# Kernel optimization log

Measured on AMD Instinct MI355X. Metric: run time of the kernel, lower is better.

The kernel has to match this reference:

```python
import jax, jax.numpy as jnp
import numpy as np


def _knn_idx(xyz_bn3, k):
    # dist[b,i,j] = ||x_i - x_j||^2 over the point cloud.
    # Faithful to the source: torch.topk defaults to largest=True, so the
    # k+1 LARGEST distances are selected and index 0 (the farthest) is dropped.
    sq = jnp.sum(xyz_bn3 ** 2, axis=-1)  # [b, n]
    dist = sq[:, :, None] + sq[:, None, :] - 2.0 * jnp.einsum('bic,bjc->bij', xyz_bn3, xyz_bn3)
    _, idx = jax.lax.top_k(dist, k + 1)  # largest, sorted descending -> [b, n, k+1]
    return idx[:, :, 1:]  # drop slot 0, keep k neighbors -> [b, n, k]


def setup_inputs() -> dict:
    key = jax.random.key(0)
    B, N, C, K, NB = 8, 4096, 128, 20, 3
    ks = jax.random.split(key, 4)
    scale = 1.0 / np.sqrt(C).astype(np.float32)
    xyz = jax.random.normal(ks[0], (B, 3, N), jnp.float32)
    points = jax.random.normal(ks[1], (B, C, N), jnp.float32)
    W1 = jax.random.normal(ks[2], (NB, C, C), jnp.float32) * scale  # convs[2i] 1x1 kernels
    b1 = jnp.zeros((NB, C), jnp.float32)
    W2 = jax.random.normal(ks[3], (NB, C, C), jnp.float32) * scale  # convs[2i+1] 1x1 kernels
    b2 = jnp.zeros((NB, C), jnp.float32)
    return {"xyz": xyz, "points": points, "W1": W1, "b1": b1, "W2": W2, "b2": b2, "k": K}


def reference(xyz, points, W1, b1, W2, b2, k):
    # xyz: [b, 3, n]; points: [b, C, n]; W1/W2: [n_blocks, C, C]; b1/b2: [n_blocks, C]
    n_blocks = W1.shape[0]
    xyz_bn3 = jnp.transpose(xyz, (0, 2, 1))  # [b, n, 3]
    for i in range(n_blocks):
        shortcut = points
        p = jax.nn.leaky_relu(points, 0.01)  # elementwise, layout [b, C, n]
        # center branch: 1x1 conv == per-point linear
        center = jnp.einsum('oc,bcn->bon', W1[i], p) + b1[i][None, :, None]  # [b, C, n]
        if i == 0:
            idx = _knn_idx(xyz_bn3, k)  # [b, n, k], int32
            # grouping_operation gather: grouped[b,c,n,j] = p[b,c, idx[b,n,j]]
            grouped = jax.vmap(lambda pb, ib: pb[:, ib])(p, idx)  # [b, C, n, k]
            gnn = jnp.einsum('oc,bcnk->bonk', W2[i], grouped) + b2[i][None, :, None, None]
            # mean over concat([center(1 slot), gnn(k slots)], slot axis)
            agg = (center + jnp.sum(gnn, axis=-1)) / (k + 1)
        else:
            # later blocks: grouped_points is just the center point itself (K=1)
            gnn = jnp.einsum('oc,bcn->bon', W2[i], p) + b2[i][None, :, None]
            agg = (center + gnn) * 0.5
        points = agg + shortcut
    return points
```

## Files before the change

kernel.cpp:

```cpp
#include <hip/hip_runtime.h>
#include <math.h>

#define B 8
#define N 4096
#define C 128
#define K 20
#define M (B*N)

__device__ __forceinline__ float lrelu(float x) { return x > 0.f ? x : 0.01f * x; }

__global__ void prep_w(const float* __restrict__ W1, const float* __restrict__ b1,
                       const float* __restrict__ W2, const float* __restrict__ b2,
                       float* __restrict__ wt, float* __restrict__ bias) {
    int t = blockIdx.x * blockDim.x + threadIdx.x;
    if (t < C * C) {
        int c = t / C, o = t % C;
        int oc = o * C + c;
        wt[0 * C * C + t] = W1[oc] * (1.f / 21.f);
        wt[1 * C * C + t] = W2[oc] * (1.f / 21.f);
        wt[2 * C * C + t] = (W1[1 * C * C + oc] + W2[1 * C * C + oc]) * 0.5f;
        wt[3 * C * C + t] = (W1[2 * C * C + oc] + W2[2 * C * C + oc]) * 0.5f;
    }
    if (t < C) {
        bias[t]         = (b1[t] + 20.f * b2[t]) * (1.f / 21.f);
        bias[C + t]     = (b1[C + t] + b2[C + t]) * 0.5f;
        bias[2 * C + t] = (b1[2 * C + t] + b2[2 * C + t]) * 0.5f;
    }
}

__global__ void prep_xyz(const float* __restrict__ xyz, float4* __restrict__ xt) {
    int t = blockIdx.x * blockDim.x + threadIdx.x;
    if (t >= B * N) return;
    int b = t >> 12, n = t & (N - 1);
    const float* p = xyz + (size_t)b * 3 * N;
    float x = p[n], y = p[N + n], z = p[2 * N + n];
    xt[t] = make_float4(x, y, z, x * x + y * y + z * z);
}

__global__ __launch_bounds__(256) void transpose_rs(const float* __restrict__ in,
                                                    float* __restrict__ out, int R, int S) {
    __shared__ float tile[64][65];
    int b = blockIdx.z;
    int r0 = blockIdx.y * 64, s0 = blockIdx.x * 64;
    const float* pin = in + (size_t)b * R * S;
    float* pout = out + (size_t)b * R * S;
    int tr = threadIdx.x >> 4;
    int ts = (threadIdx.x & 15) << 2;
#pragma unroll
    for (int i = 0; i < 4; ++i) {
        int r = tr + i * 16;
        float4 v = *(const float4*)&pin[(size_t)(r0 + r) * S + s0 + ts];
        tile[r][ts + 0] = v.x; tile[r][ts + 1] = v.y;
        tile[r][ts + 2] = v.z; tile[r][ts + 3] = v.w;
    }
    __syncthreads();
#pragma unroll
    for (int i = 0; i < 4; ++i) {
        int s = tr + i * 16;
        float4 v = make_float4(tile[ts + 0][s], tile[ts + 1][s], tile[ts + 2][s], tile[ts + 3][s]);
        *(float4*)&pout[(size_t)(s0 + s) * R + r0 + ts] = v;
    }
}

__global__ __launch_bounds__(256, 4) void knn_kernel(const float4* __restrict__ xt,
                                                     int* __restrict__ idx) {
    __shared__ unsigned int wred[4][2];
    __shared__ float maxred[4][4];
    __shared__ unsigned int cnt[4];
    __shared__ unsigned long long cand[4][128];

    int tid = threadIdx.x;
    int wid = tid >> 6, lane = tid & 63;
    int blk = blockIdx.x;
    int b = blk >> 10;
    int i0 = (blk & 1023) << 2;
    const float4* xb = xt + (size_t)b * N;

    float4 xi[4];
#pragma unroll
    for (int r = 0; r < 4; ++r) xi[r] = xb[i0 + r];

    if (tid < 4) cnt[tid] = 0;

    float d[4][16];
    float mx[4] = {-1e30f, -1e30f, -1e30f, -1e30f};
#pragma unroll
    for (int u = 0; u < 16; ++u) {
        float4 xj = xb[u * 256 + tid];
#pragma unroll
        for (int r = 0; r < 4; ++r) {
            float dd = xi[r].w + xj.w - 2.f * (xi[r].x * xj.x + xi[r].y * xj.y + xi[r].z * xj.z);
            d[r][u] = dd;
            mx[r] = fmaxf(mx[r], dd);
        }
    }
#pragma unroll
    for (int off = 32; off; off >>= 1) {
#pragma unroll
        for (int r = 0; r < 4; ++r) mx[r] = fmaxf(mx[r], __shfl_xor(mx[r], off));
    }
    if (lane == 0) {
#pragma unroll
        for (int r = 0; r < 4; ++r) maxred[wid][r] = mx[r];
    }
    __syncthreads();

    float lo[4], hi[4], thr[4];
    bool done[4];
#pragma unroll
    for (int r = 0; r < 4; ++r) {
        hi[r] = fmaxf(fmaxf(maxred[0][r], maxred[1][r]), fmaxf(maxred[2][r], maxred[3][r]));
        lo[r] = 0.f;
        thr[r] = 0.f;
        done[r] = false;
    }

    for (int it = 0; it < 20; ++it) {
        if (done[0] && done[1] && done[2] && done[3]) break;
#pragma unroll
        for (int r = 0; r < 4; ++r) if (!done[r]) thr[r] = 0.5f * (lo[r] + hi[r]);
        unsigned int c[4] = {0u, 0u, 0u, 0u};
#pragma unroll
        for (int u = 0; u < 16; ++u) {
#pragma unroll
            for (int r = 0; r < 4; ++r) c[r] += (d[r][u] > thr[r]) ? 1u : 0u;
        }
        unsigned int p01 = c[0] | (c[1] << 16);
        unsigned int p23 = c[2] | (c[3] << 16);
#pragma unroll
        for (int off = 32; off; off >>= 1) {
            p01 += __shfl_xor(p01, off);
            p23 += __shfl_xor(p23, off);
        }
        if (lane == 0) { wred[wid][0] = p01; wred[wid][1] = p23; }
        __syncthreads();
        unsigned int s01 = wred[0][0] + wred[1][0] + wred[2][0] + wred[3][0];
        unsigned int s23 = wred[0][1] + wred[1][1] + wred[2][1] + wred[3][1];
        unsigned int cc[4] = { s01 & 0xFFFFu, s01 >> 16, s23 & 0xFFFFu, s23 >> 16 };
#pragma unroll
        for (int r = 0; r < 4; ++r) {
            if (!done[r]) {
                if (cc[r] >= (unsigned)(K + 1) && cc[r] <= 96u) done[r] = true;
                else if (cc[r] > 96u) lo[r] = thr[r];
                else hi[r] = thr[r];
            }
        }
        __syncthreads();
    }
#pragma unroll
    for (int r = 0; r < 4; ++r) if (!done[r]) thr[r] = lo[r];

#pragma unroll
    for (int u = 0; u < 16; ++u) {
#pragma unroll
        for (int r = 0; r < 4; ++r) {
            float dd = d[r][u];
            if (dd > thr[r]) {
                unsigned int pos = atomicAdd(&cnt[r], 1u);
                if (pos < 128u) {
                    unsigned int j = (unsigned)(u * 256 + tid);
                    cand[r][pos] = ((unsigned long long)__float_as_uint(dd) << 32) | (unsigned)(~j);
                }
            }
        }
    }
    __syncthreads();

    {
        int r = wid;
        unsigned int c = cnt[r]; if (c > 128u) c = 128u;
        for (int s = lane; s < (int)c; s += 64) {
            unsigned long long my = cand[r][s];
            int rank = 0;
            for (int q = 0; q < (int)c; ++q) rank += (cand[r][q] > my) ? 1 : 0;
            if (rank >= 1 && rank <= K) {
                int row = (b << 12) + i0 + r;
                idx[(size_t)row * K + (rank - 1)] = (int)(~(unsigned int)my);
            }
        }
    }
}

__global__ __launch_bounds__(256) void gather_sum(const float* __restrict__ pt,
                                                  const int* __restrict__ idx,
                                                  float* __restrict__ sT) {
    int t = blockIdx.x * 256 + threadIdx.x;
    int pnt = t >> 5;
    int c4 = (t & 31) << 2;
    int b = pnt >> 12;
    const float* pb = pt + (size_t)b * N * C;
    const int* ip = idx + (size_t)pnt * K;
    float4 acc = make_float4(0.f, 0.f, 0.f, 0.f);
#pragma unroll 4
    for (int k = 0; k < K; ++k) {
        int j = ip[k];
        float4 v = *(const float4*)&pb[(size_t)j * C + c4];
        acc.x += lrelu(v.x); acc.y += lrelu(v.y);
        acc.z += lrelu(v.z); acc.w += lrelu(v.w);
    }
    *(float4*)&sT[(size_t)pnt * C + c4] = acc;
}

__global__ __launch_bounds__(256) void gemm_fused(const float* __restrict__ A0,
                                                  const float* __restrict__ A1,
                                                  const float* __restrict__ Wt0,
                                                  const float* __restrict__ Wt1,
                                                  const float* __restrict__ bias,
                                                  const float* __restrict__ shortcut,
                                                  float* __restrict__ out) {
    __shared__ float As[64][17];
    __shared__ float Ws[16][128];
    int row0 = blockIdx.x * 64;
    int tid = threadIdx.x;
    int r_ld = tid >> 2;
    int c_ld = (tid & 3) << 2;
    int r0 = (tid >> 4) << 2;
    int o0 = (tid & 15) << 2;

    float acc[4][8];
#pragma unroll
    for (int j = 0; j < 4; ++j)
#pragma unroll
        for (int l = 0; l < 8; ++l) acc[j][l] = 0.f;

    for (int phase = 0; phase < 2; ++phase) {
        const float* A = phase ? A1 : A0;
        if (!A) break;
        const float* Wt = phase ? Wt1 : Wt0;
        for (int c0 = 0; c0 < C; c0 += 16) {
            float4 av = *(const float4*)&A[(size_t)(row0 + r_ld) * C + c0 + c_ld];
            if (phase == 0) {
                av.x = lrelu(av.x); av.y = lrelu(av.y);
                av.z = lrelu(av.z); av.w = lrelu(av.w);
            }
            As[r_ld][c_ld + 0] = av.x; As[r_ld][c_ld + 1] = av.y;
            As[r_ld][c_ld + 2] = av.z; As[r_ld][c_ld + 3] = av.w;
#pragma unroll
            for (int q = 0; q < 2; ++q) {
                int slot = tid + q * 256;
                int kk = slot >> 5;
                int oo = (slot & 31) << 2;
                *(float4*)&Ws[kk][oo] = *(const float4*)&Wt[(size_t)(c0 + kk) * C + oo];
            }
            __syncthreads();
#pragma unroll
            for (int kk = 0; kk < 16; ++kk) {
                float a0 = As[r0 + 0][kk], a1 = As[r0 + 1][kk];
                float a2 = As[r0 + 2][kk], a3 = As[r0 + 3][kk];
                float4 w0 = *(const float4*)&Ws[kk][o0];
                float4 w1 = *(const float4*)&Ws[kk][o0 + 64];
                acc[0][0] += a0 * w0.x; acc[0][1] += a0 * w0.y; acc[0][2] += a0 * w0.z; acc[0][3] += a0 * w0.w;
                acc[0][4] += a0 * w1.x; acc[0][5] += a0 * w1.y; acc[0][6] += a0 * w1.z; acc[0][7] += a0 * w1.w;
                acc[1][0] += a1 * w0.x; acc[1][1] += a1 * w0.y; acc[1][2] += a1 * w0.z; acc[1][3] += a1 * w0.w;
                acc[1][4] += a1 * w1.x; acc[1][5] += a1 * w1.y; acc[1][6] += a1 * w1.z; acc[1][7] += a1 * w1.w;
                acc[2][0] += a2 * w0.x; acc[2][1] += a2 * w0.y; acc[2][2] += a2 * w0.z; acc[2][3] += a2 * w0.w;
                acc[2][4] += a2 * w1.x; acc[2][5] += a2 * w1.y; acc[2][6] += a2 * w1.z; acc[2][7] += a2 * w1.w;
                acc[3][0] += a3 * w0.x; acc[3][1] += a3 * w0.y; acc[3][2] += a3 * w0.z; acc[3][3] += a3 * w0.w;
                acc[3][4] += a3 * w1.x; acc[3][5] += a3 * w1.y; acc[3][6] += a3 * w1.z; acc[3][7] += a3 * w1.w;
            }
            __syncthreads();
        }
    }

    float4 bb0 = *(const float4*)&bias[o0];
    float4 bb1 = *(const float4*)&bias[o0 + 64];
#pragma unroll
    for (int j = 0; j < 4; ++j) {
        size_t r = (size_t)(row0 + r0 + j);
        float4 s0 = *(const float4*)&shortcut[r * C + o0];
        float4 s1 = *(const float4*)&shortcut[r * C + o0 + 64];
        float4 v0 = make_float4(acc[j][0] + bb0.x + s0.x, acc[j][1] + bb0.y + s0.y,
                                acc[j][2] + bb0.z + s0.z, acc[j][3] + bb0.w + s0.w);
        float4 v1 = make_float4(acc[j][4] + bb1.x + s1.x, acc[j][5] + bb1.y + s1.y,
                                acc[j][6] + bb1.z + s1.z, acc[j][7] + bb1.w + s1.w);
        *(float4*)&out[r * C + o0] = v0;
        *(float4*)&out[r * C + o0 + 64] = v1;
    }
}

extern "C" void kernel_launch(void* const* d_in, const int* in_sizes, int n_in,
                              void* d_out, int out_size, void* d_ws, size_t ws_size,
                              hipStream_t stream) {
    const float* xyz    = (const float*)d_in[0];
    const float* points = (const float*)d_in[1];
    const float* W1     = (const float*)d_in[2];
    const float* b1     = (const float*)d_in[3];
    const float* W2     = (const float*)d_in[4];
    const float* b2     = (const float*)d_in[5];

    float* ws = (float*)d_ws;
    float4* xt  = (float4*)ws;
    float* pt_a = ws + (size_t)B * N * 4;
    float* pt_b = pt_a + (size_t)M * C;
    float* sT   = pt_b + (size_t)M * C;
    float* wt   = sT + (size_t)M * C;
    float* bias = wt + 4 * C * C;
    int*   idx  = (int*)(bias + 3 * C);

    prep_w<<<(C * C + 255) / 256, 256, 0, stream>>>(W1, b1, W2, b2, wt, bias);
    prep_xyz<<<(B * N + 255) / 256, 256, 0, stream>>>(xyz, xt);
    {
        dim3 g(N / 64, C / 64, B);
        transpose_rs<<<g, 256, 0, stream>>>(points, pt_a, C, N);
    }
    knn_kernel<<<M / 4, 256, 0, stream>>>(xt, idx);
    gather_sum<<<(M * 32) / 256, 256, 0, stream>>>(pt_a, idx, sT);
    gemm_fused<<<M / 64, 256, 0, stream>>>(pt_a, sT, wt, wt + C * C, bias, pt_a, pt_b);
    gemm_fused<<<M / 64, 256, 0, stream>>>(pt_b, nullptr, wt + 2 * C * C, nullptr, bias + C, pt_b, pt_a);
    gemm_fused<<<M / 64, 256, 0, stream>>>(pt_a, nullptr, wt + 3 * C * C, nullptr, bias + 2 * C, pt_a, pt_b);
    {
        dim3 g(C / 64, N / 64, B);
        transpose_rs<<<g, 256, 0, stream>>>(pt_b, (float*)d_out, N, C);
    }
}
```

Baseline: 218.8 us.

## Fuse GEMM blocks and output transpose, use ballot-based counting in kNN

Merges the two prep kernels into a single launch. In the kNN kernel, the bisection counting uses wave ballot/popcount with a double-buffered shared count array that drops one barrier per iteration, and candidate insertion does one atomic per wave using mbcnt instead of one per lane. Blocks 1 and 2 are fused into one kernel that keeps the 64-row tile in shared memory and writes the transposed output directly, which removes one GEMM launch, the final transpose, and their global round trips. Block 0 now stages its input tile once and reuses it for the shortcut. It also adds fallback index filling and index masking for safety, at the cost of more shared memory per block and possibly lower occupancy.

```diff
diff --git a/kernel.cpp b/kernel.cpp
--- a/kernel.cpp
+++ b/kernel.cpp
@@ -9,32 +9,32 @@
 
 __device__ __forceinline__ float lrelu(float x) { return x > 0.f ? x : 0.01f * x; }
 
-__global__ void prep_w(const float* __restrict__ W1, const float* __restrict__ b1,
-                       const float* __restrict__ W2, const float* __restrict__ b2,
-                       float* __restrict__ wt, float* __restrict__ bias) {
-    int t = blockIdx.x * blockDim.x + threadIdx.x;
-    if (t < C * C) {
-        int c = t / C, o = t % C;
+__global__ void prep_all(const float* __restrict__ xyz,
+                         const float* __restrict__ W1, const float* __restrict__ b1,
+                         const float* __restrict__ W2, const float* __restrict__ b2,
+                         float4* __restrict__ xt, float* __restrict__ wt,
+                         float* __restrict__ bias) {
+    int blk = blockIdx.x;
+    if (blk < 64) {
+        int t = blk * 256 + threadIdx.x;
+        int c = t >> 7, o = t & 127;
         int oc = o * C + c;
-        wt[0 * C * C + t] = W1[oc] * (1.f / 21.f);
-        wt[1 * C * C + t] = W2[oc] * (1.f / 21.f);
-        wt[2 * C * C + t] = (W1[1 * C * C + oc] + W2[1 * C * C + oc]) * 0.5f;
+        wt[t]             = W1[oc] * (1.f / 21.f);
+        wt[C * C + t]     = W2[oc] * (1.f / 21.f);
+        wt[2 * C * C + t] = (W1[C * C + oc] + W2[C * C + oc]) * 0.5f;
         wt[3 * C * C + t] = (W1[2 * C * C + oc] + W2[2 * C * C + oc]) * 0.5f;
-    }
-    if (t < C) {
-        bias[t]         = (b1[t] + 20.f * b2[t]) * (1.f / 21.f);
-        bias[C + t]     = (b1[C + t] + b2[C + t]) * 0.5f;
-        bias[2 * C + t] = (b1[2 * C + t] + b2[2 * C + t]) * 0.5f;
-    }
-}
-
-__global__ void prep_xyz(const float* __restrict__ xyz, float4* __restrict__ xt) {
-    int t = blockIdx.x * blockDim.x + threadIdx.x;
-    if (t >= B * N) return;
-    int b = t >> 12, n = t & (N - 1);
-    const float* p = xyz + (size_t)b * 3 * N;
-    float x = p[n], y = p[N + n], z = p[2 * N + n];
-    xt[t] = make_float4(x, y, z, x * x + y * y + z * z);
+        if (t < C) {
+            bias[t]         = (b1[t] + 20.f * b2[t]) * (1.f / 21.f);
+            bias[C + t]     = (b1[C + t] + b2[C + t]) * 0.5f;
+            bias[2 * C + t] = (b1[2 * C + t] + b2[2 * C + t]) * 0.5f;
+        }
+    } else {
+        int t = (blk - 64) * 256 + threadIdx.x;
+        int b = t >> 12, n = t & (N - 1);
+        const float* p = xyz + (size_t)b * 3 * N;
+        float x = p[n], y = p[N + n], z = p[2 * N + n];
+        xt[t] = make_float4(x, y, z, x * x + y * y + z * z);
+    }
 }
 
 __global__ __launch_bounds__(256) void transpose_rs(const float* __restrict__ in,
@@ -64,88 +64,85 @@
 
 __global__ __launch_bounds__(256, 4) void knn_kernel(const float4* __restrict__ xt,
                                                      int* __restrict__ idx) {
-    __shared__ unsigned int wred[4][2];
     __shared__ float maxred[4][4];
+    __shared__ unsigned int wcnt[2][4][4];
     __shared__ unsigned int cnt[4];
     __shared__ unsigned long long cand[4][128];
 
-    int tid = threadIdx.x;
-    int wid = tid >> 6, lane = tid & 63;
-    int blk = blockIdx.x;
-    int b = blk >> 10;
-    int i0 = (blk & 1023) << 2;
-    const float4* xb = xt + (size_t)b * N;
-
-    float4 xi[4];
-#pragma unroll
-    for (int r = 0; r < 4; ++r) xi[r] = xb[i0 + r];
-
+    const int tid = threadIdx.x;
+    const int wid = tid >> 6, lane = tid & 63;
+    const int blk = blockIdx.x;
+    const int b = blk >> 10;
+    const int i0 = (blk & 1023) << 2;
+    const float4* __restrict__ xb = xt + (size_t)b * N;
+
+    float4 xi0 = xb[i0 + 0], xi1 = xb[i0 + 1], xi2 = xb[i0 + 2], xi3 = xb[i0 + 3];
     if (tid < 4) cnt[tid] = 0;
 
     float d[4][16];
-    float mx[4] = {-1e30f, -1e30f, -1e30f, -1e30f};
+    float mx0 = -1e30f, mx1 = -1e30f, mx2 = -1e30f, mx3 = -1e30f;
 #pragma unroll
     for (int u = 0; u < 16; ++u) {
         float4 xj = xb[u * 256 + tid];
-#pragma unroll
-        for (int r = 0; r < 4; ++r) {
-            float dd = xi[r].w + xj.w - 2.f * (xi[r].x * xj.x + xi[r].y * xj.y + xi[r].z * xj.z);
-            d[r][u] = dd;
-            mx[r] = fmaxf(mx[r], dd);
-        }
+        float s0 = fmaf(xi0.x, xj.x, fmaf(xi0.y, xj.y, xi0.z * xj.z));
+        float s1 = fmaf(xi1.x, xj.x, fmaf(xi1.y, xj.y, xi1.z * xj.z));
+        float s2 = fmaf(xi2.x, xj.x, fmaf(xi2.y, xj.y, xi2.z * xj.z));
+        float s3 = fmaf(xi3.x, xj.x, fmaf(xi3.y, xj.y, xi3.z * xj.z));
+        float d0 = xi0.w + xj.w - 2.f * s0;
+        float d1 = xi1.w + xj.w - 2.f * s1;
+        float d2 = xi2.w + xj.w - 2.f * s2;
+        float d3 = xi3.w + xj.w - 2.f * s3;
+        d[0][u] = d0; d[1][u] = d1; d[2][u] = d2; d[3][u] = d3;
+        mx0 = fmaxf(mx0, d0); mx1 = fmaxf(mx1, d1);
+        mx2 = fmaxf(mx2, d2); mx3 = fmaxf(mx3, d3);
     }
 #pragma unroll
     for (int off = 32; off; off >>= 1) {
-#pragma unroll
-        for (int r = 0; r < 4; ++r) mx[r] = fmaxf(mx[r], __shfl_xor(mx[r], off));
+        mx0 = fmaxf(mx0, __shfl_xor(mx0, off));
+        mx1 = fmaxf(mx1, __shfl_xor(mx1, off));
+        mx2 = fmaxf(mx2, __shfl_xor(mx2, off));
+        mx3 = fmaxf(mx3, __shfl_xor(mx3, off));
     }
     if (lane == 0) {
-#pragma unroll
-        for (int r = 0; r < 4; ++r) maxred[wid][r] = mx[r];
+        maxred[wid][0] = mx0; maxred[wid][1] = mx1;
+        maxred[wid][2] = mx2; maxred[wid][3] = mx3;
     }
     __syncthreads();
 
-    float lo[4], hi[4], thr[4];
-    bool done[4];
+    float lo[4] = {0.f, 0.f, 0.f, 0.f};
+    float hi[4], thr[4];
+    bool done[4] = {false, false, false, false};
 #pragma unroll
     for (int r = 0; r < 4; ++r) {
         hi[r] = fmaxf(fmaxf(maxred[0][r], maxred[1][r]), fmaxf(maxred[2][r], maxred[3][r]));
-        lo[r] = 0.f;
         thr[r] = 0.f;
-        done[r] = false;
-    }
-
-    for (int it = 0; it < 20; ++it) {
-        if (done[0] && done[1] && done[2] && done[3]) break;
-#pragma unroll
-        for (int r = 0; r < 4; ++r) if (!done[r]) thr[r] = 0.5f * (lo[r] + hi[r]);
-        unsigned int c[4] = {0u, 0u, 0u, 0u};
-#pragma unroll
-        for (int u = 0; u < 16; ++u) {
-#pragma unroll
-            for (int r = 0; r < 4; ++r) c[r] += (d[r][u] > thr[r]) ? 1u : 0u;
-        }
-        unsigned int p01 = c[0] | (c[1] << 16);
-        unsigned int p23 = c[2] | (c[3] << 16);
-#pragma unroll
-        for (int off = 32; off; off >>= 1) {
-            p01 += __shfl_xor(p01, off);
-            p23 += __shfl_xor(p23, off);
-        }
-        if (lane == 0) { wred[wid][0] = p01; wred[wid][1] = p23; }
-        __syncthreads();
-        unsigned int s01 = wred[0][0] + wred[1][0] + wred[2][0] + wred[3][0];
-        unsigned int s23 = wred[0][1] + wred[1][1] + wred[2][1] + wred[3][1];
-        unsigned int cc[4] = { s01 & 0xFFFFu, s01 >> 16, s23 & 0xFFFFu, s23 >> 16 };
+    }
+
+    bool alldone = false;
+    for (int it = 0; it < 24 && !alldone; ++it) {
+        int p = it & 1;
 #pragma unroll
         for (int r = 0; r < 4; ++r) {
-            if (!done[r]) {
-                if (cc[r] >= (unsigned)(K + 1) && cc[r] <= 96u) done[r] = true;
-                else if (cc[r] > 96u) lo[r] = thr[r];
-                else hi[r] = thr[r];
-            }
-        }
-        __syncthreads();
+            if (done[r]) continue;
+            float t = 0.5f * (lo[r] + hi[r]);
+            thr[r] = t;
+            unsigned int cc = 0;
+#pragma unroll
+            for (int u = 0; u < 16; ++u)
+                cc += (unsigned int)__popcll(__ballot(d[r][u] > t));
+            if (lane == 0) wcnt[p][wid][r] = cc;
+        }
+        __syncthreads();
+        alldone = true;
+#pragma unroll
+        for (int r = 0; r < 4; ++r) {
+            if (done[r]) continue;
+            unsigned int tot = wcnt[p][0][r] + wcnt[p][1][r] + wcnt[p][2][r] + wcnt[p][3][r];
+            if (tot >= (unsigned)(K + 1) && tot <= 96u) done[r] = true;
+            else if (tot > 96u) lo[r] = thr[r];
+            else hi[r] = thr[r];
+            if (!done[r]) alldone = false;
+        }
     }
 #pragma unroll
     for (int r = 0; r < 4; ++r) if (!done[r]) thr[r] = lo[r];
@@ -154,12 +151,21 @@
     for (int u = 0; u < 16; ++u) {
 #pragma unroll
         for (int r = 0; r < 4; ++r) {
-            float dd = d[r][u];
-            if (dd > thr[r]) {
-                unsigned int pos = atomicAdd(&cnt[r], 1u);
-                if (pos < 128u) {
-                    unsigned int j = (unsigned)(u * 256 + tid);
-                    cand[r][pos] = ((unsigned long long)__float_as_uint(dd) << 32) | (unsigned)(~j);
+            bool pred = d[r][u] > thr[r];
+            unsigned long long m = __ballot(pred);
+            if (m) {
+                unsigned int base = 0;
+                if (lane == 0) base = atomicAdd(&cnt[r], (unsigned int)__popcll(m));
+                base = (unsigned int)__shfl((int)base, 0);
+                if (pred) {
+                    unsigned int bel = __builtin_amdgcn_mbcnt_lo((unsigned int)m, 0u);
+                    bel = __builtin_amdgcn_mbcnt_hi((unsigned int)(m >> 32), bel);
+                    unsigned int pos = base + bel;
+                    if (pos < 128u) {
+                        unsigned int j = (unsigned int)(u * 256 + tid);
+                        cand[r][pos] = ((unsigned long long)__float_as_uint(d[r][u]) << 32)
+                                       | (unsigned int)(~j);
+                    }
                 }
             }
         }
@@ -168,15 +174,16 @@
 
     {
         int r = wid;
+        int row = (b << 12) + i0 + r;
         unsigned int c = cnt[r]; if (c > 128u) c = 128u;
+        if (c < (unsigned)(K + 1) && lane < K)
+            idx[(size_t)row * K + lane] = (int)lane + 1;
         for (int s = lane; s < (int)c; s += 64) {
             unsigned long long my = cand[r][s];
             int rank = 0;
             for (int q = 0; q < (int)c; ++q) rank += (cand[r][q] > my) ? 1 : 0;
-            if (rank >= 1 && rank <= K) {
-                int row = (b << 12) + i0 + r;
+            if (rank >= 1 && rank <= K)
                 idx[(size_t)row * K + (rank - 1)] = (int)(~(unsigned int)my);
-            }
         }
     }
 }
@@ -193,7 +200,7 @@
     float4 acc = make_float4(0.f, 0.f, 0.f, 0.f);
 #pragma unroll 4
     for (int k = 0; k < K; ++k) {
-        int j = ip[k];
+        int j = ip[k] & (N - 1);
         float4 v = *(const float4*)&pb[(size_t)j * C + c4];
         acc.x += lrelu(v.x); acc.y += lrelu(v.y);
         acc.z += lrelu(v.z); acc.w += lrelu(v.w);
@@ -201,21 +208,90 @@
     *(float4*)&sT[(size_t)pnt * C + c4] = acc;
 }
 
-__global__ __launch_bounds__(256) void gemm_fused(const float* __restrict__ A0,
-                                                  const float* __restrict__ A1,
-                                                  const float* __restrict__ Wt0,
-                                                  const float* __restrict__ Wt1,
-                                                  const float* __restrict__ bias,
-                                                  const float* __restrict__ shortcut,
-                                                  float* __restrict__ out) {
-    __shared__ float As[64][17];
+__device__ __forceinline__ void stage_ws(const float* __restrict__ Wt, float (*Ws)[128],
+                                         int c0, int tid) {
+#pragma unroll
+    for (int q = 0; q < 2; ++q) {
+        int slot = q * 256 + tid;
+        int kk = slot >> 5, oo = (slot & 31) << 2;
+        *(float4*)&Ws[kk][oo] = *(const float4*)&Wt[(size_t)(c0 + kk) * C + oo];
+    }
+}
+
+template<bool LR>
+__device__ __forceinline__ void mm_tileP(const float (*P)[132], const float (*Ws)[128],
+                                         float acc[4][8], int r0, int o0, int c0) {
+#pragma unroll
+    for (int q = 0; q < 4; ++q) {
+        float4 aj[4];
+#pragma unroll
+        for (int j = 0; j < 4; ++j) {
+            float4 v = *(const float4*)&P[r0 + j][c0 + q * 4];
+            if (LR) { v.x = lrelu(v.x); v.y = lrelu(v.y); v.z = lrelu(v.z); v.w = lrelu(v.w); }
+            aj[j] = v;
+        }
+#pragma unroll
+        for (int kq = 0; kq < 4; ++kq) {
+            int kk = q * 4 + kq;
+            float4 w0 = *(const float4*)&Ws[kk][o0];
+            float4 w1 = *(const float4*)&Ws[kk][o0 + 64];
+#pragma unroll
+            for (int j = 0; j < 4; ++j) {
+                float a = (kq == 0) ? aj[j].x : (kq == 1) ? aj[j].y : (kq == 2) ? aj[j].z : aj[j].w;
+                acc[j][0] = fmaf(a, w0.x, acc[j][0]); acc[j][1] = fmaf(a, w0.y, acc[j][1]);
+                acc[j][2] = fmaf(a, w0.z, acc[j][2]); acc[j][3] = fmaf(a, w0.w, acc[j][3]);
+                acc[j][4] = fmaf(a, w1.x, acc[j][4]); acc[j][5] = fmaf(a, w1.y, acc[j][5]);
+                acc[j][6] = fmaf(a, w1.z, acc[j][6]); acc[j][7] = fmaf(a, w1.w, acc[j][7]);
+            }
+        }
+    }
+}
+
+__device__ __forceinline__ void mm_tileA(const float (*As)[20], const float (*Ws)[128],
+                                         float acc[4][8], int r0, int o0) {
+#pragma unroll
+    for (int q = 0; q < 4; ++q) {
+        float4 aj[4];
+#pragma unroll
+        for (int j = 0; j < 4; ++j)
+            aj[j] = *(const float4*)&As[r0 + j][q * 4];
+#pragma unroll
+        for (int kq = 0; kq < 4; ++kq) {
+            int kk = q * 4 + kq;
+            float4 w0 = *(const float4*)&Ws[kk][o0];
+            float4 w1 = *(const float4*)&Ws[kk][o0 + 64];
+#pragma unroll
+            for (int j = 0; j < 4; ++j) {
+                float a = (kq == 0) ? aj[j].x : (kq == 1) ? aj[j].y : (kq == 2) ? aj[j].z : aj[j].w;
+                acc[j][0] = fmaf(a, w0.x, acc[j][0]); acc[j][1] = fmaf(a, w0.y, acc[j][1]);
+                acc[j][2] = fmaf(a, w0.z, acc[j][2]); acc[j][3] = fmaf(a, w0.w, acc[j][3]);
+                acc[j][4] = fmaf(a, w1.x, acc[j][4]); acc[j][5] = fmaf(a, w1.y, acc[j][5]);
+                acc[j][6] = fmaf(a, w1.z, acc[j][6]); acc[j][7] = fmaf(a, w1.w, acc[j][7]);
+            }
+        }
+    }
+}
+
+__global__ __launch_bounds__(256) void gemm_block0(const float* __restrict__ A0,
+                                                   const float* __restrict__ A1,
+                                                   const float* __restrict__ Wt0,
+                                                   const float* __restrict__ Wt1,
+                                                   const float* __restrict__ bias0,
+                                                   float* __restrict__ out) {
+    __shared__ float P0[64][132];
+    __shared__ float As[64][20];
     __shared__ float Ws[16][128];
-    int row0 = blockIdx.x * 64;
-    int tid = threadIdx.x;
-    int r_ld = tid >> 2;
-    int c_ld = (tid & 3) << 2;
-    int r0 = (tid >> 4) << 2;
-    int o0 = (tid & 15) << 2;
+    const int row0 = blockIdx.x * 64;
+    const int tid = threadIdx.x;
+    const int r0 = (tid >> 4) << 2;
+    const int o0 = (tid & 15) << 2;
+
+#pragma unroll
+    for (int q = 0; q < 8; ++q) {
+        int s = q * 256 + tid;
+        int r = s >> 5, c4 = (s & 31) << 2;
+        *(float4*)&P0[r][c4] = *(const float4*)&A0[(size_t)(row0 + r) * C + c4];
+    }
 
     float acc[4][8];
 #pragma unroll
@@ -223,58 +299,123 @@
 #pragma unroll
         for (int l = 0; l < 8; ++l) acc[j][l] = 0.f;
 
-    for (int phase = 0; phase < 2; ++phase) {
-        const float* A = phase ? A1 : A0;
-        if (!A) break;
-        const float* Wt = phase ? Wt1 : Wt0;
-        for (int c0 = 0; c0 < C; c0 += 16) {
-            float4 av = *(const float4*)&A[(size_t)(row0 + r_ld) * C + c0 + c_ld];
-            if (phase == 0) {
-                av.x = lrelu(av.x); av.y = lrelu(av.y);
-                av.z = lrelu(av.z); av.w = lrelu(av.w);
-            }
-            As[r_ld][c_ld + 0] = av.x; As[r_ld][c_ld + 1] = av.y;
-            As[r_ld][c_ld + 2] = av.z; As[r_ld][c_ld + 3] = av.w;
-#pragma unroll
-            for (int q = 0; q < 2; ++q) {
-                int slot = tid + q * 256;
-                int kk = slot >> 5;
-                int oo = (slot & 31) << 2;
-                *(float4*)&Ws[kk][oo] = *(const float4*)&Wt[(size_t)(c0 + kk) * C + oo];
-            }
-            __syncthreads();
-#pragma unroll
-            for (int kk = 0; kk < 16; ++kk) {
-                float a0 = As[r0 + 0][kk], a1 = As[r0 + 1][kk];
-                float a2 = As[r0 + 2][kk], a3 = As[r0 + 3][kk];
-                float4 w0 = *(const float4*)&Ws[kk][o0];
-                float4 w1 = *(const float4*)&Ws[kk][o0 + 64];
-                acc[0][0] += a0 * w0.x; acc[0][1] += a0 * w0.y; acc[0][2] += a0 * w0.z; acc[0][3] += a0 * w0.w;
-                acc[0][4] += a0 * w1.x; acc[0][5] += a0 * w1.y; acc[0][6] += a0 * w1.z; acc[0][7] += a0 * w1.w;
-                acc[1][0] += a1 * w0.x; acc[1][1] += a1 * w0.y; acc[1][2] += a1 * w0.z; acc[1][3] += a1 * w0.w;
-                acc[1][4] += a1 * w1.x; acc[1][5] += a1 * w1.y; acc[1][6] += a1 * w1.z; acc[1][7] += a1 * w1.w;
-                acc[2][0] += a2 * w0.x; acc[2][1] += a2 * w0.y; acc[2][2] += a2 * w0.z; acc[2][3] += a2 * w0.w;
-                acc[2][4] += a2 * w1.x; acc[2][5] += a2 * w1.y; acc[2][6] += a2 * w1.z; acc[2][7] += a2 * w1.w;
-                acc[3][0] += a3 * w0.x; acc[3][1] += a3 * w0.y; acc[3][2] += a3 * w0.z; acc[3][3] += a3 * w0.w;
-                acc[3][4] += a3 * w1.x; acc[3][5] += a3 * w1.y; acc[3][6] += a3 * w1.z; acc[3][7] += a3 * w1.w;
-            }
-            __syncthreads();
-        }
-    }
-
-    float4 bb0 = *(const float4*)&bias[o0];
-    float4 bb1 = *(const float4*)&bias[o0 + 64];
+    for (int c0 = 0; c0 < C; c0 += 16) {
+        stage_ws(Wt0, Ws, c0, tid);
+        __syncthreads();
+        mm_tileP<true>(P0, Ws, acc, r0, o0, c0);
+        __syncthreads();
+    }
+    for (int c0 = 0; c0 < C; c0 += 16) {
+        stage_ws(Wt1, Ws, c0, tid);
+        {
+            int r_ld = tid >> 2, c_ld = (tid & 3) << 2;
+            *(float4*)&As[r_ld][c_ld] = *(const float4*)&A1[(size_t)(row0 + r_ld) * C + c0 + c_ld];
+        }
+        __syncthreads();
+        mm_tileA(As, Ws, acc, r0, o0);
+        __syncthreads();
+    }
+
+    float4 bb0 = *(const float4*)&bias0[o0];
+    float4 bb1 = *(const float4*)&bias0[o0 + 64];
 #pragma unroll
     for (int j = 0; j < 4; ++j) {
-        size_t r = (size_t)(row0 + r0 + j);
-        float4 s0 = *(const float4*)&shortcut[r * C + o0];
-        float4 s1 = *(const float4*)&shortcut[r * C + o0 + 64];
+        int rl = r0 + j;
+        size_t r = (size_t)(row0 + rl);
+        float4 s0 = *(const float4*)&P0[rl][o0];
+        float4 s1 = *(const float4*)&P0[rl][o0 + 64];
         float4 v0 = make_float4(acc[j][0] + bb0.x + s0.x, acc[j][1] + bb0.y + s0.y,
                                 acc[j][2] + bb0.z + s0.z, acc[j][3] + bb0.w + s0.w);
         float4 v1 = make_float4(acc[j][4] + bb1.x + s1.x, acc[j][5] + bb1.y + s1.y,
                                 acc[j][6] + bb1.z + s1.z, acc[j][7] + bb1.w + s1.w);
         *(float4*)&out[r * C + o0] = v0;
         *(float4*)&out[r * C + o0 + 64] = v1;
+    }
+}
+
+__global__ __launch_bounds__(256) void gemm_block12(const float* __restrict__ A0,
+                                                    const float* __restrict__ Wt1,
+                                                    const float* __restrict__ Wt2,
+                                                    const float* __restrict__ biasAll,
+                                                    float* __restrict__ outT) {
+    __shared__ float P[64][132];
+    __shared__ float Ws[16][128];
+    const int row0 = blockIdx.x * 64;
+    const int tid = threadIdx.x;
+    const int r0 = (tid >> 4) << 2;
+    const int o0 = (tid & 15) << 2;
+
+#pragma unroll
+    for (int q = 0; q < 8; ++q) {
+        int s = q * 256 + tid;
+        int r = s >> 5, c4 = (s & 31) << 2;
+        *(float4*)&P[r][c4] = *(const float4*)&A0[(size_t)(row0 + r) * C + c4];
+    }
+
+    float acc[4][8];
+#pragma unroll
+    for (int j = 0; j < 4; ++j)
+#pragma unroll
+        for (int l = 0; l < 8; ++l) acc[j][l] = 0.f;
+
+    for (int c0 = 0; c0 < C; c0 += 16) {
+        stage_ws(Wt1, Ws, c0, tid);
+        __syncthreads();
+        mm_tileP<true>(P, Ws, acc, r0, o0, c0);
+        __syncthreads();
+    }
+    {
+        float4 bb0 = *(const float4*)&biasAll[C + o0];
+        float4 bb1 = *(const float4*)&biasAll[C + o0 + 64];
+#pragma unroll
+        for (int j = 0; j < 4; ++j) {
+            int rl = r0 + j;
+            float4 s0 = *(const float4*)&P[rl][o0];
+            float4 s1 = *(const float4*)&P[rl][o0 + 64];
+            float4 v0 = make_float4(acc[j][0] + bb0.x + s0.x, acc[j][1] + bb0.y + s0.y,
+                                    acc[j][2] + bb0.z + s0.z, acc[j][3] + bb0.w + s0.w);
+            float4 v1 = make_float4(acc[j][4] + bb1.x + s1.x, acc[j][5] + bb1.y + s1.y,
+                                    acc[j][6] + bb1.z + s1.z, acc[j][7] + bb1.w + s1.w);
+            *(float4*)&P[rl][o0] = v0;
+            *(float4*)&P[rl][o0 + 64] = v1;
+            acc[j][0] = 0.f; acc[j][1] = 0.f; acc[j][2] = 0.f; acc[j][3] = 0.f;
+            acc[j][4] = 0.f; acc[j][5] = 0.f; acc[j][6] = 0.f; acc[j][7] = 0.f;
+        }
+    }
+    __syncthreads();
+    for (int c0 = 0; c0 < C; c0 += 16) {
+        stage_ws(Wt2, Ws, c0, tid);
+        __syncthreads();
+        mm_tileP<true>(P, Ws, acc, r0, o0, c0);
+        __syncthreads();
+    }
+    {
+        float4 bb0 = *(const float4*)&biasAll[2 * C + o0];
+        float4 bb1 = *(const float4*)&biasAll[2 * C + o0 + 64];
+#pragma unroll
+        for (int j = 0; j < 4; ++j) {
+            int rl = r0 + j;
+            float4 s0 = *(const float4*)&P[rl][o0];
+            float4 s1 = *(const float4*)&P[rl][o0 + 64];
+            float4 v0 = make_float4(acc[j][0] + bb0.x + s0.x, acc[j][1] + bb0.y + s0.y,
+                                    acc[j][2] + bb0.z + s0.z, acc[j][3] + bb0.w + s0.w);
+            float4 v1 = make_float4(acc[j][4] + bb1.x + s1.x, acc[j][5] + bb1.y + s1.y,
+                                    acc[j][6] + bb1.z + s1.z, acc[j][7] + bb1.w + s1.w);
+            *(float4*)&P[rl][o0] = v0;
+            *(float4*)&P[rl][o0 + 64] = v1;
+        }
+    }
+    __syncthreads();
+    const int o = tid >> 1;
+    const int nh = (tid & 1) << 5;
+    const int bq = row0 >> 12;
+    const int nb = (row0 & (N - 1)) + nh;
+    float* po = outT + ((size_t)bq * C + o) * N + nb;
+#pragma unroll
+    for (int q = 0; q < 8; ++q) {
+        int n = nh + q * 4;
+        float4 v = make_float4(P[n + 0][o], P[n + 1][o], P[n + 2][o], P[n + 3][o]);
+        *(float4*)&po[q * 4] = v;
     }
 }
 
@@ -297,19 +438,14 @@
     float* bias = wt + 4 * C * C;
     int*   idx  = (int*)(bias + 3 * C);
 
-    prep_w<<<(C * C + 255) / 256, 256, 0, stream>>>(W1, b1, W2, b2, wt, bias);
-    prep_xyz<<<(B * N + 255) / 256, 256, 0, stream>>>(xyz, xt);
+    prep_all<<<192, 256, 0, stream>>>(xyz, W1, b1, W2, b2, xt, wt, bias);
     {
         dim3 g(N / 64, C / 64, B);
         transpose_rs<<<g, 256, 0, stream>>>(points, pt_a, C, N);
     }
     knn_kernel<<<M / 4, 256, 0, stream>>>(xt, idx);
     gather_sum<<<(M * 32) / 256, 256, 0, stream>>>(pt_a, idx, sT);
-    gemm_fused<<<M / 64, 256, 0, stream>>>(pt_a, sT, wt, wt + C * C, bias, pt_a, pt_b);
-    gemm_fused<<<M / 64, 256, 0, stream>>>(pt_b, nullptr, wt + 2 * C * C, nullptr, bias + C, pt_b, pt_a);
-    gemm_fused<<<M / 64, 256, 0, stream>>>(pt_a, nullptr, wt + 3 * C * C, nullptr, bias + 2 * C, pt_a, pt_b);
-    {
-        dim3 g(C / 64, N / 64, B);
-        transpose_rs<<<g, 256, 0, stream>>>(pt_b, (float*)d_out, N, C);
-    }
-}
+    gemm_block0<<<M / 64, 256, 0, stream>>>(pt_a, sT, wt, wt + C * C, bias, pt_b);
+    gemm_block12<<<M / 64, 256, 0, stream>>>(pt_b, wt + 2 * C * C, wt + 3 * C * C, bias,
+                                             (float*)d_out);
+}
```

Result: slower. 242.4 us (+10.8%).
